# Kernel optimization log

Measured on AMD Instinct MI355X. Metric: run time of the kernel, lower is better.

## Reference

```python
import jax, jax.numpy as jnp
import numpy as np

N = 10000; E = 320000; NFEAT = 500; NHID = 256; C = 16; K = 64
GAMMA = 4; ALPHA = 0.1; BETA = 1.0; EPS = 0.1; LAMDA = 0.5; W1 = 0.5

def _init(key, shape, scale=0.05):
    return jax.random.normal(key, shape, dtype=jnp.float32) * scale

def setup_inputs():
    key = jax.random.key(0)
    ks = jax.random.split(key, 24)
    return {
        "x": jax.random.normal(ks[0], (N, NFEAT), dtype=jnp.float32),
        "edge_index": jax.random.randint(ks[1], (2, E), 0, N),
        "edge_weight": jax.random.uniform(ks[2], (E,), dtype=jnp.float32),
        "adj_weight": jax.random.uniform(ks[3], (E,), dtype=jnp.float32),
        "connect": jax.random.uniform(ks[4], (N, N), dtype=jnp.float32),
        "confidence_in": jax.random.uniform(ks[5], (2, E), dtype=jnp.float32),
        "lin1_w": _init(ks[6], (NHID, NFEAT)),
        "lin1_b": jnp.zeros((NHID,), jnp.float32),
        "lin2_w": _init(ks[7], (C, NHID)),
        "lin2_b": jnp.zeros((C,), jnp.float32),
        "lin_a_w": _init(ks[8], (NHID, N), 0.01),
        "lin_a_b": jnp.zeros((NHID,), jnp.float32),
        "lin_n_w": _init(ks[9], (C, C)),
        "lin_n_b": jnp.zeros((C,), jnp.float32),
        "left_w": _init(ks[10], (C, C)),
        "att_w": _init(ks[11], (1, C)),
        "v_w": _init(ks[12], (K, NHID)),
        "v_b": jnp.zeros((K,), jnp.float32),
        "W": _init(ks[13], (C, C)),
        "conf_param": jnp.zeros((3,), jnp.float32),
        "b_param": jnp.zeros((1,), jnp.float32),
    }

def _forward(x, edge_index, edge_weight, adj_weight, connect, confidence_in,
             lin1_w, lin1_b, lin2_w, lin2_b, lin_a_w, lin_a_b, lin_n_w, lin_n_b,
             left_w, att_w, v_w, v_b, W, conf_param, b_param):
    row, col = edge_index[0], edge_index[1]

    def spmm(vals, out_idx, M):
        # COO sparse @ dense: scatter-add per-edge vals * gathered rows of M
        return jax.ops.segment_sum(vals[:, None] * M, out_idx, num_segments=N)

    x_a = connect @ lin_a_w.T + lin_a_b            # [N, NHID]
    h = x @ lin1_w.T + lin1_b
    h = jax.nn.relu((1.0 - LAMDA) * h + LAMDA * x_a)
    raw = h                                        # [N, NHID]
    h = h @ lin2_w.T + lin2_b                      # [N, C]

    # neighbor label distribution: row-normalized adj @ one_hot(argmax softmax)
    y_hat = jnp.argmax(jax.nn.softmax(h, axis=1), axis=1)
    one_hot = jax.nn.one_hot(y_hat, C, dtype=h.dtype)
    nei = spmm(adj_weight, row, one_hot[col])
    s = nei.sum(axis=1, keepdims=True)
    nei = jnp.where(s != 0, nei / jnp.where(s == 0, 1.0, s), 0.0)

    x_n = jax.nn.relu(nei @ lin_n_w.T + lin_n_b)
    h = (1.0 - W1) * h + W1 * x_n
    init = h

    # per-edge attention-based confidence mixed with input confidences
    lx = h @ left_w.T
    confi = jax.nn.relu(lx[row] + lx[col])
    confi = jax.nn.sigmoid((confi @ att_w.T)[:, 0])
    w = jax.nn.softmax(conf_param)
    conf = confi * w[0] + confidence_in[0] * w[1] + confidence_in[1] * w[2]  # [E]

    V = raw @ v_w.T + v_b                          # [N, K]
    U = spmm(adj_weight, row, V[col]) @ jnp.linalg.inv(V.T @ V)
    eyeK = jnp.eye(K, dtype=h.dtype)

    def edge_mask_score(score):
        S = score ** 2
        ss = jnp.sort(S)
        q1, q3 = ss[E // 4], ss[3 * E // 4]
        thr = (q3 + 1.5 * (q3 - q1)) * conf        # [E]
        mask = (S < thr).astype(h.dtype)
        return (score + b_param[0]) * mask

    def update_u(U, V):
        SS = edge_mask_score(edge_weight - jnp.sum(U[row] * V[col], axis=1))
        temp = spmm(SS, row, V[col]) + U @ (V.T @ V) + EPS * (h @ (h.T @ V))
        inver = jnp.linalg.inv((1.0 + EPS) * (V.T @ V) + BETA * eyeK)
        return temp @ inver

    def update_v(U, V):
        SS = edge_mask_score(edge_weight - jnp.sum(V[row] * U[col], axis=1))
        # A^T @ U: scatter over col with U[row]
        temp = spmm(SS, col, U[row]) + V @ (U.T @ U) + EPS * (h @ (h.T @ U))
        inver = jnp.linalg.inv((1.0 + EPS) * (U.T @ U) + BETA * eyeK)
        return temp @ inver

    for j in range(GAMMA):
        if j % 2 == 0:
            U = update_u(U, V)
        else:
            V = update_v(U, V)

    prop = U @ (h.T @ V).T                         # [N, C]
    out = (1.0 - ALPHA) * prop + ALPHA * init
    return out @ W

def reference(x, edge_index, edge_weight, adj_weight, connect, confidence_in,
              lin1_w, lin1_b, lin2_w, lin2_b, lin_a_w, lin_a_b, lin_n_w, lin_n_b,
              left_w, att_w, v_w, v_b, W, conf_param, b_param):
    return _forward(x, edge_index, edge_weight, adj_weight, connect, confidence_in,
                    lin1_w, lin1_b, lin2_w, lin2_b, lin_a_w, lin_a_b, lin_n_w, lin_n_b,
                    left_w, att_w, v_w, v_b, W, conf_param, b_param)
```

## Files before the change

kernel.cpp:

```cpp
#include <hip/hip_runtime.h>
#include <cstddef>
#include <cstdint>


constexpr int kN  = 10000;
constexpr int kE  = 320000;
constexpr int kNH = 256;
constexpr int kC  = 16;
constexpr int kK  = 64;
constexpr int GRAM_PARTS = 256;
constexpr int PHASE_BLOCKS = 768;

struct SelState {
  int bin1[2]; int rem1[2];
};

typedef short bf16x8 __attribute__((ext_vector_type(8)));
typedef float f32x4 __attribute__((ext_vector_type(4)));
typedef ushort ushort8 __attribute__((ext_vector_type(8)));

__device__ __forceinline__ ushort f2bf(float x) {
  unsigned u = __float_as_uint(x);
  unsigned r = (u + 0x7fffu + ((u >> 16) & 1u)) >> 16;
  return (ushort)r;
}
__device__ __forceinline__ float bf2f(ushort h) {
  return __uint_as_float((unsigned)h << 16);
}
__device__ __forceinline__ int swz(int row, int byteInRow) {
  int chunk = (byteInRow >> 4) ^ ((row >> 1) & 3);
  return row * 64 + (chunk << 4) + (byteInRow & 15);
}

__global__ void split3_bf(const float* __restrict__ Wa, ushort* ha, ushort* la,
                          const float* __restrict__ Wx, ushort* hx, ushort* lx2,
                          const float* __restrict__ Wv, ushort* hv, ushort* lv)
{
  const int n1 = 256 * 10016, n2 = 256 * 512, n3 = 64 * 256;
  int t = blockIdx.x * 256 + threadIdx.x;
  if (t < n1) {
    int r = t / 10016, c = t % 10016;
    float v = (c < 10000) ? Wa[(size_t)r * 10000 + c] : 0.f;
    ushort h = f2bf(v); ha[t] = h; la[t] = f2bf(v - bf2f(h));
  } else if (t < n1 + n2) {
    int q = t - n1;
    int r = q / 512, c = q % 512;
    float v = (c < 500) ? Wx[(size_t)r * 500 + c] : 0.f;
    ushort h = f2bf(v); hx[q] = h; lx2[q] = f2bf(v - bf2f(h));
  } else if (t < n1 + n2 + n3) {
    int q = t - n1 - n2;
    float v = Wv[q];
    ushort h = f2bf(v); hv[q] = h; lv[q] = f2bf(v - bf2f(h));
  }
}

template<int BN, bool ALO>
__global__ __launch_bounds__(256) void gemm_v3(
    const float* __restrict__ A, const ushort* __restrict__ Bhg,
    const ushort* __restrict__ Blg, const float* __restrict__ bias,
    float* __restrict__ out, int M, int K, int Kp, int KR, int outStride)
{
  __shared__ __align__(16) char sAh[64 * 64];
  __shared__ __align__(16) char sAl[ALO ? 64 * 64 : 16];
  __shared__ __align__(16) char sBh[BN * 64];
  __shared__ __align__(16) char sBl[BN * 64];
  const int t = threadIdx.x;
  const int lane = t & 63, w = t >> 6;
  const int bm = blockIdx.x * 64;
  const int k0 = blockIdx.z * KR;
  const int kend = min(K, k0 + KR);
  out += (size_t)blockIdx.z * M * outStride;
  constexpr int WN = BN / 64;
  constexpr int RB = WN;
  const int wc = (w % WN) * 64;
  const int wr = (w / WN) * (RB * 16);
  const int l15 = lane & 15;
  const int lByte = (lane >> 4) * 16;
  const int ar = t >> 2, ac = t & 3;

  float pv[8];
  ushort8 pbh[WN], pbl[WN];

  {
    int gr = bm + ar, gk = k0 + ac * 8;
    if (gr < M && gk + 8 <= kend) {
      float4 v0 = *reinterpret_cast<const float4*>(A + (size_t)gr * K + gk);
      float4 v1 = *reinterpret_cast<const float4*>(A + (size_t)gr * K + gk + 4);
      pv[0] = v0.x; pv[1] = v0.y; pv[2] = v0.z; pv[3] = v0.w;
      pv[4] = v1.x; pv[5] = v1.y; pv[6] = v1.z; pv[7] = v1.w;
    } else {
#pragma unroll
      for (int q = 0; q < 8; q++)
        pv[q] = (gr < M && gk + q < kend) ? A[(size_t)gr * K + gk + q] : 0.f;
    }
#pragma unroll
    for (int i2 = 0; i2 < WN; i2++) {
      int idx = t + i2 * 256;
      int r = idx >> 2, c = idx & 3;
      size_t gb = (size_t)r * Kp + k0 + c * 8;
      pbh[i2] = *reinterpret_cast<const ushort8*>(Bhg + gb);
      pbl[i2] = *reinterpret_cast<const ushort8*>(Blg + gb);
    }
  }

  f32x4 acc[RB][4] = {};
  for (int kt = k0; kt < kend; kt += 32) {
    {
      ushort8 h8, l8;
#pragma unroll
      for (int q = 0; q < 8; q++) {
        ushort h = f2bf(pv[q]); h8[q] = h;
        if (ALO) l8[q] = f2bf(pv[q] - bf2f(h));
      }
      *reinterpret_cast<ushort8*>(sAh + swz(ar, ac * 16)) = h8;
      if (ALO) *reinterpret_cast<ushort8*>(sAl + swz(ar, ac * 16)) = l8;
#pragma unroll
      for (int i2 = 0; i2 < WN; i2++) {
        int idx = t + i2 * 256;
        int r = idx >> 2, c = idx & 3;
        *reinterpret_cast<ushort8*>(sBh + swz(r, c * 16)) = pbh[i2];
        *reinterpret_cast<ushort8*>(sBl + swz(r, c * 16)) = pbl[i2];
      }
    }
    __syncthreads();
    int kn = kt + 32;
    if (kn < kend) {
      int gr = bm + ar, gk = kn + ac * 8;
      if (gr < M && gk + 8 <= kend) {
        float4 v0 = *reinterpret_cast<const float4*>(A + (size_t)gr * K + gk);
        float4 v1 = *reinterpret_cast<const float4*>(A + (size_t)gr * K + gk + 4);
        pv[0] = v0.x; pv[1] = v0.y; pv[2] = v0.z; pv[3] = v0.w;
        pv[4] = v1.x; pv[5] = v1.y; pv[6] = v1.z; pv[7] = v1.w;
      } else {
#pragma unroll
        for (int q = 0; q < 8; q++)
          pv[q] = (gr < M && gk + q < kend) ? A[(size_t)gr * K + gk + q] : 0.f;
      }
#pragma unroll
      for (int i2 = 0; i2 < WN; i2++) {
        int idx = t + i2 * 256;
        int r = idx >> 2, c = idx & 3;
        size_t gb = (size_t)r * Kp + kn + c * 8;
        pbh[i2] = *reinterpret_cast<const ushort8*>(Bhg + gb);
        pbl[i2] = *reinterpret_cast<const ushort8*>(Blg + gb);
      }
    }
    bf16x8 bh[4], bl[4];
#pragma unroll
    for (int nbq = 0; nbq < 4; nbq++) {
      int rr = wc + nbq * 16 + l15;
      bh[nbq] = *reinterpret_cast<const bf16x8*>(sBh + swz(rr, lByte));
      bl[nbq] = *reinterpret_cast<const bf16x8*>(sBl + swz(rr, lByte));
    }
#pragma unroll
    for (int rb = 0; rb < RB; rb++) {
      int rr = wr + rb * 16 + l15;
      bf16x8 ah = *reinterpret_cast<const bf16x8*>(sAh + swz(rr, lByte));
#pragma unroll
      for (int nbq = 0; nbq < 4; nbq++) {
        acc[rb][nbq] = __builtin_amdgcn_mfma_f32_16x16x32_bf16(ah, bh[nbq], acc[rb][nbq], 0, 0, 0);
        acc[rb][nbq] = __builtin_amdgcn_mfma_f32_16x16x32_bf16(ah, bl[nbq], acc[rb][nbq], 0, 0, 0);
      }
      if (ALO) {
        bf16x8 al = *reinterpret_cast<const bf16x8*>(sAl + swz(rr, lByte));
#pragma unroll
        for (int nbq = 0; nbq < 4; nbq++)
          acc[rb][nbq] = __builtin_amdgcn_mfma_f32_16x16x32_bf16(al, bh[nbq], acc[rb][nbq], 0, 0, 0);
      }
    }
    __syncthreads();
  }
#pragma unroll
  for (int rb = 0; rb < RB; rb++) {
#pragma unroll
    for (int nbq = 0; nbq < 4; nbq++) {
      int colg = wc + nbq * 16 + l15;
      float bv = bias ? bias[colg] : 0.f;
#pragma unroll
      for (int jj = 0; jj < 4; jj++) {
        int rowg = bm + wr + rb * 16 + (lane >> 4) * 4 + jj;
        if (rowg < M) out[(size_t)rowg * outStride + colg] = acc[rb][nbq][jj] + bv;
      }
    }
  }
}

__global__ void reduce_raw(const float4* __restrict__ Pa, const float4* px,
                           const float* __restrict__ ba, const float* __restrict__ b1,
                           float4* rawOut, int* cntR, int* cntC, int* fillR,
                           int* fillC, float* nei)
{
  int t = blockIdx.x * 256 + threadIdx.x;
  if (t < kN) { cntR[t] = 0; cntC[t] = 0; fillR[t] = 0; fillC[t] = 0; }
  if (t < kN * kC) nei[t] = 0.f;
  if (t >= kN * kNH / 4) return;
  const int sl = kN * kNH / 4;
  float4 s = Pa[t];
#pragma unroll
  for (int p = 1; p < 6; p++) {
    float4 q = Pa[t + (size_t)p * sl];
    s.x += q.x; s.y += q.y; s.z += q.z; s.w += q.w;
  }
  float4 pxv = px[t];
  int c4 = t & 63;
  float4 vba = reinterpret_cast<const float4*>(ba)[c4];
  float4 vb1 = reinterpret_cast<const float4*>(b1)[c4];
  float4 r;
  r.x = fmaxf(0.5f * (s.x + vba.x) + 0.5f * (pxv.x + vb1.x), 0.f);
  r.y = fmaxf(0.5f * (s.y + vba.y) + 0.5f * (pxv.y + vb1.y), 0.f);
  r.z = fmaxf(0.5f * (s.z + vba.z) + 0.5f * (pxv.z + vb1.z), 0.f);
  r.w = fmaxf(0.5f * (s.w + vba.w) + 0.5f * (pxv.w + vb1.w), 0.f);
  rawOut[t] = r;
}

struct MegaArgs {
  const float* raw;
  const float* lin2_w; const float* lin2_b;
  const int* row; const int* col;
  const float* aw; const float* ew;
  const float* lnw; const float* lnb;
  const float* left_w; const float* att_w;
  const float* ci; const float* conf_p; const float* b_param;
  const float* Wm;
  float* h16; int* yhat; float* nei; float* hC; float* lx; float* conf;
  int* cntR; int* cntC; int* fillR; int* fillC; int* startR; int* startC;
  int* eR; int* eC; int* othR; int* othC;
  float* Va; float* Vb; float* Ua; float* Ub; float* T;
  float* score; float* G; float* Gi; float* Gp; float* hTX; float* Hp;
  int* hist1; int* h2a; int* h2b;
  float* P;
  SelState* sel;
  float* out;
};

__device__ __forceinline__ void uv_at(const MegaArgs& a, int j,
                                      float*& Ucur, float*& Unxt,
                                      float*& Vcur, float*& Vnxt)
{
  int uU = (j >= 1) + (j >= 3);
  int uV = (j >= 2) + (j >= 4);
  Ucur = (uU & 1) ? a.Ub : a.Ua; Unxt = (uU & 1) ? a.Ua : a.Ub;
  Vcur = (uV & 1) ? a.Vb : a.Va; Vnxt = (uV & 1) ? a.Va : a.Vb;
}

__device__ void gram2_dev(const float* M, const float* hc, float* P, int b, float* shm)
{
  float* sM = shm;
  float* sH = shm + 512;
  const int t = threadIdx.x;
  const int aG = t >> 2, cG0 = (t & 3) * 16;
  const int aH = t >> 4, cH0 = (t & 15) * 4;
  float accG[16]; float accH[4];
#pragma unroll
  for (int q = 0; q < 16; q++) accG[q] = 0.f;
#pragma unroll
  for (int q = 0; q < 4; q++) accH[q] = 0.f;
  int r0 = b * 40, r1 = min(kN, r0 + 40);
  for (int rb = r0; rb < r1; rb += 8) {
    int nb2 = min(8, r1 - rb);
    __syncthreads();
    for (int q = t; q < nb2 * 64; q += 256) sM[q] = M[(size_t)rb * 64 + q];
    for (int q = t; q < nb2 * 16; q += 256) sH[q] = hc[(size_t)rb * 16 + q];
    __syncthreads();
    for (int r = 0; r < nb2; r++) {
      float avG = sM[r * 64 + aG];
      const float* sbG = &sM[r * 64 + cG0];
#pragma unroll
      for (int q = 0; q < 16; q++) accG[q] += avG * sbG[q];
      float avH = sH[r * 16 + aH];
      const float* sbH = &sM[r * 64 + cH0];
#pragma unroll
      for (int q = 0; q < 4; q++) accH[q] += avH * sbH[q];
    }
  }
  float* p1 = P + (size_t)b * 5120 + aG * 64 + cG0;
#pragma unroll
  for (int q = 0; q < 16; q++) p1[q] = accG[q];
  float* p2 = P + (size_t)b * 5120 + 4096 + aH * 64 + cH0;
#pragma unroll
  for (int q = 0; q < 4; q++) p2[q] = accH[q];
}

__device__ void inverse_dev(const float* G, float* Gi, float alpha, float beta,
                            const float* hTX, float* Gp, float* Hp, float* shm)
{
  float* A = shm;
  float* prow = shm + 8448;
  float* fcol = shm + 8576;
  const int t = threadIdx.x;
  for (int q = t; q < 64 * 128; q += 256) {
    int r = q >> 7, c = q & 127;
    float v;
    if (c < 64) v = alpha * G[r * 64 + c] + ((c == r) ? beta : 0.f);
    else        v = (c - 64 == r) ? 1.f : 0.f;
    A[r * 132 + c] = v;
  }
  __syncthreads();
  const int i  = t >> 2;
  const int c0 = (t & 3) * 32;
  for (int k = 0; k < 64; k++) {
    if (t < 128) prow[t] = A[k * 132 + t];
    else if (t < 192) fcol[t - 128] = A[(t - 128) * 132 + k];
    __syncthreads();
    float pinv = 1.f / prow[k];
    float f = fcol[i];
    float4* Ar = reinterpret_cast<float4*>(&A[i * 132 + c0]);
    const float4* pr = reinterpret_cast<const float4*>(&prow[c0]);
    if (i == k) {
#pragma unroll
      for (int q = 0; q < 8; q++) {
        float4 p = pr[q];
        p.x *= pinv; p.y *= pinv; p.z *= pinv; p.w *= pinv;
        Ar[q] = p;
      }
    } else {
#pragma unroll
      for (int q = 0; q < 8; q++) {
        float4 p = pr[q]; float4 av = Ar[q];
        av.x -= f * (p.x * pinv); av.y -= f * (p.y * pinv);
        av.z -= f * (p.z * pinv); av.w -= f * (p.w * pinv);
        Ar[q] = av;
      }
    }
    __syncthreads();
  }
  for (int q = t; q < 4096; q += 256) Gi[q] = A[(q >> 6) * 132 + 64 + (q & 63)];
  if (Gp) {
    for (int q = t; q < 4096; q += 256) {
      int r = q >> 6, k = q & 63;
      float s = 0.f;
#pragma unroll 8
      for (int jj = 0; jj < 64; jj++) s += G[r * 64 + jj] * A[jj * 132 + 64 + k];
      Gp[q] = s;
    }
    for (int q = t; q < 1024; q += 256) {
      int c = q >> 6, k = q & 63;
      float s = 0.f;
#pragma unroll 8
      for (int jj = 0; jj < 64; jj++) s += hTX[c * 64 + jj] * A[jj * 132 + 64 + k];
      Hp[q] = 0.1f * s;
    }
  }
}

__device__ void scan_core(const int* H, int R, int* shm, int outSlot)
{
  const int t = threadIdx.x;
  int* part = shm;
  const int4* H4 = reinterpret_cast<const int4*>(H + t * 256);
  int lsum = 0;
  for (int b = 0; b < 64; b++) { int4 v = H4[b]; lsum += v.x + v.y + v.z + v.w; }
  part[t] = lsum;
  __syncthreads();
  for (int off = 1; off < 256; off <<= 1) {
    int v = part[t];
    int u = (t >= off) ? part[t - off] : 0;
    __syncthreads();
    part[t] = v + u;
    __syncthreads();
  }
  int cum = part[t] - lsum;
  int fb = -1, fr = 0;
  for (int b = 0; b < 64; b++) {
    int4 v = H4[b];
    int bb = t * 256 + b * 4;
    if (fb < 0 && R >= cum && R < cum + v.x) { fb = bb;     fr = R - cum; } cum += v.x;
    if (fb < 0 && R >= cum && R < cum + v.y) { fb = bb + 1; fr = R - cum; } cum += v.y;
    if (fb < 0 && R >= cum && R < cum + v.z) { fb = bb + 2; fr = R - cum; } cum += v.z;
    if (fb < 0 && R >= cum && R < cum + v.w) { fb = bb + 3; fr = R - cum; } cum += v.w;
  }
  if (fb >= 0) { shm[outSlot] = fb; shm[outSlot + 1] = fr; }
  __syncthreads();
}

__device__ void spmm_dev(const float* vals, const float* score, const float* conf,
                         float thr, float bp0,
                         const int* start, const int* eids, const int* oth,
                         const float* Msrc, float* T, int wid0, int wstride)
{
  int lane = threadIdx.x & 63;
  for (int wid = wid0; wid < kN; wid += wstride) {
    int p = start[wid], pend = start[wid + 1];
    float acc = 0.f;
    for (; p + 4 <= pend; p += 4) {
      int e0 = eids[p], e1 = eids[p + 1], e2 = eids[p + 2], e3 = eids[p + 3];
      int o0 = oth[p], o1 = oth[p + 1], o2 = oth[p + 2], o3 = oth[p + 3];
      float m0 = Msrc[(size_t)o0 * 64 + lane];
      float m1 = Msrc[(size_t)o1 * 64 + lane];
      float m2 = Msrc[(size_t)o2 * 64 + lane];
      float m3 = Msrc[(size_t)o3 * 64 + lane];
      float v0, v1, v2, v3;
      if (vals) { v0 = vals[e0]; v1 = vals[e1]; v2 = vals[e2]; v3 = vals[e3]; }
      else {
        float s0 = score[e0], s1 = score[e1], s2 = score[e2], s3 = score[e3];
        v0 = (s0 * s0 < thr * conf[e0]) ? (s0 + bp0) : 0.f;
        v1 = (s1 * s1 < thr * conf[e1]) ? (s1 + bp0) : 0.f;
        v2 = (s2 * s2 < thr * conf[e2]) ? (s2 + bp0) : 0.f;
        v3 = (s3 * s3 < thr * conf[e3]) ? (s3 + bp0) : 0.f;
      }
      acc += v0 * m0 + v1 * m1 + v2 * m2 + v3 * m3;
    }
    for (; p < pend; ++p) {
      int e = eids[p];
      float v;
      if (vals) v = vals[e];
      else { float sc = score[e]; v = (sc * sc < thr * conf[e]) ? (sc + bp0) : 0.f; }
      acc += v * Msrc[(size_t)oth[p] * 64 + lane];
    }
    T[(size_t)wid * 64 + lane] = acc;
  }
}

__device__ void outf_dev(const MegaArgs& a, const float* T, const float* X,
                         float* Out, int gtid, int gsz)
{
  for (int i = gtid; i < 65536; i += gsz) { a.hist1[i] = 0; a.h2a[i] = 0; a.h2b[i] = 0; }
  for (int t = gtid; t < kN * 16; t += gsz) {
    int i = t >> 4, kq = t & 15;
    const float* ti = T + (size_t)i * 64;
    const float4* G4 = reinterpret_cast<const float4*>(a.Gi);
    float4 s = make_float4(0.f, 0.f, 0.f, 0.f);
#pragma unroll 8
    for (int jj = 0; jj < 64; jj++) {
      float tv = ti[jj];
      float4 g = G4[jj * 16 + kq];
      s.x += tv * g.x; s.y += tv * g.y; s.z += tv * g.z; s.w += tv * g.w;
    }
    if (X) {
      const float* xi = X + (size_t)i * 64;
      const float4* Gp4 = reinterpret_cast<const float4*>(a.Gp);
      float4 s2 = make_float4(0.f, 0.f, 0.f, 0.f);
#pragma unroll 8
      for (int jj = 0; jj < 64; jj++) {
        float xv = xi[jj];
        float4 g = Gp4[jj * 16 + kq];
        s2.x += xv * g.x; s2.y += xv * g.y; s2.z += xv * g.z; s2.w += xv * g.w;
      }
      s.x += s2.x; s.y += s2.y; s.z += s2.z; s.w += s2.w;
      const float4* Hp4 = reinterpret_cast<const float4*>(a.Hp);
      float4 s3 = make_float4(0.f, 0.f, 0.f, 0.f);
#pragma unroll
      for (int c = 0; c < 16; c++) {
        float hv = a.hC[(size_t)i * 16 + c];
        float4 g = Hp4[c * 16 + kq];
        s3.x += hv * g.x; s3.y += hv * g.y; s3.z += hv * g.z; s3.w += hv * g.w;
      }
      s.x += s3.x; s.y += s3.y; s.z += s3.z; s.w += s3.w;
    }
    *reinterpret_cast<float4*>(Out + (size_t)i * 64 + kq * 4) = s;
  }
}

__device__ void reduce_dev(const MegaArgs& a, int gtid, int gsz)
{
  for (int c = gtid; c < 5120; c += gsz) {
    float s = 0.f;
    for (int p = 0; p < GRAM_PARTS; p++) s += a.P[(size_t)p * 5120 + c];
    if (c < 4096) a.G[c] = s;
    else a.hTX[c - 4096] = s;
  }
}

__global__ __launch_bounds__(256, 4) void mega_phase(MegaArgs a, int phase, int j)
{
  __shared__ __align__(16) float smem[8704];
  const int tid = threadIdx.x;
  const int bid = blockIdx.x;
  const int nb  = gridDim.x;
  const int gtid = bid * 256 + tid;
  const int gsz = nb * 256;
  float *Ucur, *Unxt, *Vcur, *Vnxt;
  uv_at(a, j, Ucur, Unxt, Vcur, Vnxt);
  bool up = ((j & 1) == 0);
  const float* Ma   = up ? Ucur : Vcur;
  const float* Mb   = up ? Vcur : Ucur;
  const float* Moth = up ? Vcur : Ucur;
  const float* Xcur = up ? Ucur : Vcur;
  float* Xout       = up ? Unxt : Vnxt;

  switch (phase) {
  case 0: {
    for (int t = gtid; t < kN * 16; t += gsz) {
      int i = t >> 4, jj = t & 15;
      const float4* av4 = reinterpret_cast<const float4*>(a.raw + (size_t)i * 256);
      const float4* bv4 = reinterpret_cast<const float4*>(a.lin2_w + (size_t)jj * 256);
      float s = a.lin2_b[jj];
#pragma unroll 8
      for (int q = 0; q < 64; q++) {
        float4 av = av4[q], bv = bv4[q];
        s += av.x * bv.x + av.y * bv.y + av.z * bv.z + av.w * bv.w;
      }
      a.h16[t] = s;
      float m = s; int am = jj;
#pragma unroll
      for (int off = 1; off < 16; off <<= 1) {
        float om = __shfl_xor(m, off);
        int oa = __shfl_xor(am, off);
        if (om > m || (om == m && oa < am)) { m = om; am = oa; }
      }
      if (jj == 0) a.yhat[i] = am;
    }
  } break;
  case 1: {
    for (int e = gtid; e < kE; e += gsz) {
      int r = a.row[e], c = a.col[e];
      atomicAdd(&a.cntR[r], 1);
      atomicAdd(&a.cntC[c], 1);
      atomicAdd(&a.nei[(size_t)r * 16 + a.yhat[c]], a.aw[e]);
    }
    for (int part = bid; part < GRAM_PARTS; part += nb)
      gram2_dev(a.Va, a.Va, a.P, part, smem);
  } break;
  case 2: {
    if (bid == 0) {
      int* part = (int*)smem;
      for (int pass = 0; pass < 2; ++pass) {
        const int* cnt = pass ? a.cntC : a.cntR;
        int* start = pass ? a.startC : a.startR;
        int bbase = tid * 40;
        int s = 0;
        for (int q = 0; q < 40; q++) { int idx = bbase + q; if (idx < kN) s += cnt[idx]; }
        part[tid] = s;
        __syncthreads();
        for (int off = 1; off < 256; off <<= 1) {
          int v = part[tid];
          int u = (tid >= off) ? part[tid - off] : 0;
          __syncthreads();
          part[tid] = v + u;
          __syncthreads();
        }
        int run = part[tid] - s;
        for (int q = 0; q < 40; q++) {
          int idx = bbase + q;
          if (idx < kN) { start[idx] = run; run += cnt[idx]; }
        }
        if (tid == 255) start[kN] = part[255];
        __syncthreads();
      }
    } else {
      int g2 = (bid - 1) * 256 + tid, s2 = (nb - 1) * 256;
      for (int i = g2; i < kN; i += s2) {
        float nv[16]; float s = 0.f;
#pragma unroll
        for (int c = 0; c < 16; c++) { nv[c] = a.nei[(size_t)i * 16 + c]; s += nv[c]; }
        float inv = (s != 0.f) ? 1.f / s : 0.f;
#pragma unroll
        for (int jj = 0; jj < 16; jj++) {
          float xn = a.lnb[jj];
#pragma unroll
          for (int c = 0; c < 16; c++) xn += (nv[c] * inv) * a.lnw[jj * 16 + c];
          xn = fmaxf(xn, 0.f);
          a.hC[(size_t)i * 16 + jj] = 0.5f * a.h16[(size_t)i * 16 + jj] + 0.5f * xn;
        }
      }
      for (int c = g2; c < 5120; c += s2) {
        float s = 0.f;
        for (int p = 0; p < GRAM_PARTS; p++) s += a.P[(size_t)p * 5120 + c];
        if (c < 4096) a.G[c] = s;
        else a.hTX[c - 4096] = s;
      }
    }
  } break;
  case 3: {
    if (bid == 0) {
      inverse_dev(a.G, a.Gi, 1.0f, 0.0f, nullptr, nullptr, nullptr, smem);
    } else {
      int g2 = (bid - 1) * 256 + tid, s2 = (nb - 1) * 256;
      for (int e = g2; e < kE; e += s2) {
        int r = a.row[e], c = a.col[e];
        int pr = a.startR[r] + atomicAdd(&a.fillR[r], 1);
        a.eR[pr] = e; a.othR[pr] = c;
        int pc = a.startC[c] + atomicAdd(&a.fillC[c], 1);
        a.eC[pc] = e; a.othC[pc] = r;
      }
      for (int t = g2; t < kN * 16; t += s2) {
        int i = t >> 4, jj = t & 15;
        float s = 0.f;
#pragma unroll
        for (int c = 0; c < 16; c++) s += a.hC[(size_t)i * 16 + c] * a.left_w[jj * 16 + c];
        a.lx[t] = s;
      }
    }
  } break;
  case 4: {
    for (int e = gtid; e < kE; e += gsz) {
      float p0 = a.conf_p[0], p1 = a.conf_p[1], p2 = a.conf_p[2];
      float m = fmaxf(p0, fmaxf(p1, p2));
      float e0 = expf(p0 - m), e1 = expf(p1 - m), e2 = expf(p2 - m);
      float inv = 1.f / (e0 + e1 + e2);
      float w0 = e0 * inv, w1 = e1 * inv, w2 = e2 * inv;
      const float* aa = a.lx + (size_t)a.row[e] * 16;
      const float* bb = a.lx + (size_t)a.col[e] * 16;
      float s = 0.f;
#pragma unroll
      for (int c = 0; c < 16; c++) s += fmaxf(aa[c] + bb[c], 0.f) * a.att_w[c];
      float cf = 1.f / (1.f + expf(-s));
      a.conf[e] = cf * w0 + a.ci[e] * w1 + a.ci[(size_t)kE + e] * w2;
    }
    spmm_dev(a.aw, nullptr, nullptr, 0.f, 0.f,
             a.startR, a.eR, a.othR, a.Va, a.T, bid * 4 + (tid >> 6), nb * 4);
  } break;
  case 5: outf_dev(a, a.T, nullptr, a.Ua, gtid, gsz); break;
  case 6: {
    for (int e = gtid; e < kE; e += gsz) {
      const float4* av4 = reinterpret_cast<const float4*>(Ma + (size_t)a.row[e] * 64);
      const float4* bv4 = reinterpret_cast<const float4*>(Mb + (size_t)a.col[e] * 64);
      float s = 0.f;
#pragma unroll
      for (int q = 0; q < 16; q++) {
        float4 av = av4[q], bv = bv4[q];
        s += av.x * bv.x + av.y * bv.y + av.z * bv.z + av.w * bv.w;
      }
      float sc = a.ew[e] - s;
      a.score[e] = sc;
      unsigned u = __float_as_uint(sc * sc);
      atomicAdd(&a.hist1[u >> 16], 1);
    }
    for (int part = bid; part < GRAM_PARTS; part += nb)
      gram2_dev(Moth, a.hC, a.P, part, smem);
  } break;
  case 7: {
    reduce_dev(a, gtid, gsz);
    int* ishm = (int*)smem;
    scan_core(a.hist1, kE / 4, ishm, 256);
    int b0 = ishm[256];
    if (bid == 0 && tid == 0) { a.sel->bin1[0] = ishm[256]; a.sel->rem1[0] = ishm[257]; }
    scan_core(a.hist1, 3 * kE / 4, ishm, 258);
    int b1 = ishm[258];
    if (bid == 0 && tid == 0) { a.sel->bin1[1] = ishm[258]; a.sel->rem1[1] = ishm[259]; }
    for (int e = gtid; e < kE; e += gsz) {
      float sc = a.score[e];
      unsigned u = __float_as_uint(sc * sc);
      int top = (int)(u >> 16);
      if (top == b0) atomicAdd(&a.h2a[u & 0xFFFF], 1);
      if (top == b1) atomicAdd(&a.h2b[u & 0xFFFF], 1);
    }
  } break;
  case 8: {
    if (bid == 0) {
      inverse_dev(a.G, a.Gi, 1.1f, 1.0f, a.hTX, a.Gp, a.Hp, smem);
    } else {
      int* ishm = (int*)smem;
      int bA = a.sel->bin1[0], bB = a.sel->bin1[1];
      int rA = a.sel->rem1[0], rB = a.sel->rem1[1];
      scan_core(a.h2a, rA, ishm, 256);
      int f0 = ishm[256];
      scan_core(a.h2b, rB, ishm, 258);
      int f1 = ishm[258];
      float q1 = __uint_as_float(((unsigned)bA << 16) | (unsigned)f0);
      float q3 = __uint_as_float(((unsigned)bB << 16) | (unsigned)f1);
      float thr = q3 + 1.5f * (q3 - q1);
      float bp0 = a.b_param[0];
      if (up) spmm_dev(nullptr, a.score, a.conf, thr, bp0,
                       a.startR, a.eR, a.othR, Vcur, a.T,
                       (bid - 1) * 4 + (tid >> 6), (nb - 1) * 4);
      else    spmm_dev(nullptr, a.score, a.conf, thr, bp0,
                       a.startC, a.eC, a.othC, Ucur, a.T,
                       (bid - 1) * 4 + (tid >> 6), (nb - 1) * 4);
    }
  } break;
  case 9: outf_dev(a, a.T, Xcur, Xout, gtid, gsz); break;
  case 10: {
    for (int part = bid; part < GRAM_PARTS; part += nb)
      gram2_dev(Vcur, a.hC, a.P, part, smem);
  } break;
  case 11: reduce_dev(a, gtid, gsz); break;
  case 12: {
    float* sh = smem;
    float* sW = smem + 1024;
    for (int q = tid; q < 1024; q += 256) sh[q] = a.hTX[q];
    sW[tid] = a.Wm[tid & 255];
    __syncthreads();
    for (int i = gtid; i < kN; i += gsz) {
      const float* u = Ucur + (size_t)i * 64;
      float pre[16];
#pragma unroll
      for (int c = 0; c < 16; c++) {
        float s = 0.f;
#pragma unroll
        for (int k = 0; k < 64; k++) s += u[k] * sh[c * 64 + k];
        pre[c] = 0.9f * s + 0.1f * a.hC[(size_t)i * 16 + c];
      }
#pragma unroll
      for (int jj = 0; jj < 16; jj++) {
        float o = 0.f;
#pragma unroll
        for (int c = 0; c < 16; c++) o += pre[c] * sW[c * 16 + jj];
        a.out[(size_t)i * 16 + jj] = o;
      }
    }
  } break;
  }
}

extern "C" void kernel_launch(void* const* d_in, const int* in_sizes, int n_in,
                              void* d_out, int out_size, void* d_ws, size_t ws_size,
                              hipStream_t stream)
{
  const float* x       = (const float*)d_in[0];
  const int*   eidx    = (const int*)d_in[1];
  const float* ew      = (const float*)d_in[2];
  const float* aw      = (const float*)d_in[3];
  const float* connect = (const float*)d_in[4];
  const float* ci      = (const float*)d_in[5];
  const float* lin1_w  = (const float*)d_in[6];
  const float* lin1_b  = (const float*)d_in[7];
  const float* lin2_w  = (const float*)d_in[8];
  const float* lin2_b  = (const float*)d_in[9];
  const float* lin_a_w = (const float*)d_in[10];
  const float* lin_a_b = (const float*)d_in[11];
  const float* lin_n_w = (const float*)d_in[12];
  const float* lin_n_b = (const float*)d_in[13];
  const float* left_w  = (const float*)d_in[14];
  const float* att_w   = (const float*)d_in[15];
  const float* v_w     = (const float*)d_in[16];
  const float* v_b     = (const float*)d_in[17];
  const float* Wm      = (const float*)d_in[18];
  const float* conf_p  = (const float*)d_in[19];
  const float* b_param = (const float*)d_in[20];
  const int* row = eidx;
  const int* col = eidx + kE;
  float* out = (float*)d_out;

  char* base = (char*)d_ws;
  size_t off = 0;
  auto alloc = [&](size_t bytes) -> void* {
    void* p = base + off;
    off += bytes;
    off = (off + 255) & ~(size_t)255;
    return p;
  };
  float* raw   = (float*)alloc((size_t)kN * kNH * 4);
  float* h16   = (float*)alloc((size_t)kN * kC * 4);
  float* hC    = (float*)alloc((size_t)kN * kC * 4);
  float* nei   = (float*)alloc((size_t)kN * kC * 4);
  float* lx    = (float*)alloc((size_t)kN * kC * 4);
  int*   yhat  = (int*)alloc((size_t)kN * 4);
  float* conf  = (float*)alloc((size_t)kE * 4);
  float* Va    = (float*)alloc((size_t)kN * kK * 4);
  float* Vb    = (float*)alloc((size_t)kN * kK * 4);
  float* Ua    = (float*)alloc((size_t)kN * kK * 4);
  float* Ub    = (float*)alloc((size_t)kN * kK * 4);
  float* T     = (float*)alloc((size_t)kN * kK * 4);
  float* score = (float*)alloc((size_t)kE * 4);
  float* G     = (float*)alloc(64 * 64 * 4);
  float* Gi    = (float*)alloc(64 * 64 * 4);
  float* Gp    = (float*)alloc(64 * 64 * 4);
  float* hTX   = (float*)alloc(kC * kK * 4);
  float* Hp    = (float*)alloc(kC * kK * 4);
  int* hist1   = (int*)alloc(65536 * 4);
  int* h2a     = (int*)alloc(65536 * 4);
  int* h2b     = (int*)alloc(65536 * 4);
  SelState* sel = (SelState*)alloc(sizeof(SelState));
  int* cntR    = (int*)alloc((size_t)kN * 4);
  int* cntC    = (int*)alloc((size_t)kN * 4);
  int* fillR   = (int*)alloc((size_t)kN * 4);
  int* fillC   = (int*)alloc((size_t)kN * 4);
  int* startR  = (int*)alloc((size_t)(kN + 1) * 4);
  int* startC  = (int*)alloc((size_t)(kN + 1) * 4);
  int* eR      = (int*)alloc((size_t)kE * 4);
  int* eC      = (int*)alloc((size_t)kE * 4);
  int* othR    = (int*)alloc((size_t)kE * 4);
  int* othC    = (int*)alloc((size_t)kE * 4);
  float* P     = (float*)alloc((size_t)GRAM_PARTS * 5120 * 4);
  const int KpC = 10016, KpX = 512, KpV = 256;
  ushort* BcH = (ushort*)alloc((size_t)256 * KpC * 2);
  ushort* BcL = (ushort*)alloc((size_t)256 * KpC * 2);
  ushort* BxH = (ushort*)alloc((size_t)256 * KpX * 2);
  ushort* BxL = (ushort*)alloc((size_t)256 * KpX * 2);
  ushort* BvH = (ushort*)alloc((size_t)64 * KpV * 2);
  ushort* BvL = (ushort*)alloc((size_t)64 * KpV * 2);
  float* Pbig  = (float*)alloc((size_t)6 * kN * kNH * 4);

  {
    int total = 256 * KpC + 256 * KpX + 64 * KpV;
    split3_bf<<<(total + 255) / 256, 256, 0, stream>>>(
        lin_a_w, BcH, BcL, lin1_w, BxH, BxL, v_w, BvH, BvL);
  }

  gemm_v3<256, false><<<dim3(157, 1, 6), 256, 0, stream>>>(
      connect, BcH, BcL, nullptr, Pbig, kN, 10000, KpC, 1696, kNH);
  gemm_v3<256, true><<<dim3(157, 1, 1), 256, 0, stream>>>(
      x, BxH, BxL, nullptr, raw, kN, 500, KpX, 512, kNH);
  reduce_raw<<<(kN * kNH / 4 + 255) / 256, 256, 0, stream>>>(
      (const float4*)Pbig, (const float4*)raw, lin_a_b, lin1_b, (float4*)raw,
      cntR, cntC, fillR, fillC, nei);
  gemm_v3<64, true><<<dim3(157, 1, 1), 256, 0, stream>>>(
      raw, BvH, BvL, v_b, Va, kN, 256, KpV, 256, kK);

  MegaArgs ma;
  ma.raw = raw; ma.lin2_w = lin2_w; ma.lin2_b = lin2_b;
  ma.row = row; ma.col = col; ma.aw = aw; ma.ew = ew;
  ma.lnw = lin_n_w; ma.lnb = lin_n_b; ma.left_w = left_w; ma.att_w = att_w;
  ma.ci = ci; ma.conf_p = conf_p; ma.b_param = b_param; ma.Wm = Wm;
  ma.h16 = h16; ma.yhat = yhat; ma.nei = nei; ma.hC = hC; ma.lx = lx; ma.conf = conf;
  ma.cntR = cntR; ma.cntC = cntC; ma.fillR = fillR; ma.fillC = fillC;
  ma.startR = startR; ma.startC = startC;
  ma.eR = eR; ma.eC = eC; ma.othR = othR; ma.othC = othC;
  ma.Va = Va; ma.Vb = Vb; ma.Ua = Ua; ma.Ub = Ub; ma.T = T;
  ma.score = score; ma.G = G; ma.Gi = Gi; ma.Gp = Gp; ma.hTX = hTX; ma.Hp = Hp;
  ma.hist1 = hist1; ma.h2a = h2a; ma.h2b = h2b;
  ma.P = P; ma.sel = sel; ma.out = out;

  const dim3 pg(PHASE_BLOCKS);
  for (int p = 0; p <= 5; p++) mega_phase<<<pg, 256, 0, stream>>>(ma, p, 0);
  for (int j = 0; j < 4; j++)
    for (int p = 6; p <= 9; p++) mega_phase<<<pg, 256, 0, stream>>>(ma, p, j);
  mega_phase<<<pg, 256, 0, stream>>>(ma, 10, 4);
  mega_phase<<<pg, 256, 0, stream>>>(ma, 11, 4);
  mega_phase<<<pg, 256, 0, stream>>>(ma, 12, 4);
}
```

Baseline: 2.490 ms.

## Use two-level coarse histograms for quantile select; drop GEMM register prefetch

Adds 256-bin coarse histograms alongside the 65536-bin ones, so the quantile search first scans the coarse bins and then only one 256-entry fine slice. Previously every block in the phase read the full 64K histogram twice per scan. The cost is an extra atomic per edge into a small, highly contended coarse histogram. Separately, the GEMM drops its register double-buffer prefetch of the A and B tiles and loads each tile directly before the sync, which lowers register pressure but gives up load/compute overlap.

```diff
diff --git a/kernel.cpp b/kernel.cpp
--- a/kernel.cpp
+++ b/kernel.cpp
@@ -78,73 +78,41 @@
   const int lByte = (lane >> 4) * 16;
   const int ar = t >> 2, ac = t & 3;
 
-  float pv[8];
-  ushort8 pbh[WN], pbl[WN];
-
-  {
-    int gr = bm + ar, gk = k0 + ac * 8;
-    if (gr < M && gk + 8 <= kend) {
-      float4 v0 = *reinterpret_cast<const float4*>(A + (size_t)gr * K + gk);
-      float4 v1 = *reinterpret_cast<const float4*>(A + (size_t)gr * K + gk + 4);
-      pv[0] = v0.x; pv[1] = v0.y; pv[2] = v0.z; pv[3] = v0.w;
-      pv[4] = v1.x; pv[5] = v1.y; pv[6] = v1.z; pv[7] = v1.w;
-    } else {
-#pragma unroll
-      for (int q = 0; q < 8; q++)
-        pv[q] = (gr < M && gk + q < kend) ? A[(size_t)gr * K + gk + q] : 0.f;
-    }
-#pragma unroll
-    for (int i2 = 0; i2 < WN; i2++) {
-      int idx = t + i2 * 256;
-      int r = idx >> 2, c = idx & 3;
-      size_t gb = (size_t)r * Kp + k0 + c * 8;
-      pbh[i2] = *reinterpret_cast<const ushort8*>(Bhg + gb);
-      pbl[i2] = *reinterpret_cast<const ushort8*>(Blg + gb);
-    }
-  }
-
   f32x4 acc[RB][4] = {};
   for (int kt = k0; kt < kend; kt += 32) {
     {
-      ushort8 h8, l8;
-#pragma unroll
-      for (int q = 0; q < 8; q++) {
-        ushort h = f2bf(pv[q]); h8[q] = h;
-        if (ALO) l8[q] = f2bf(pv[q] - bf2f(h));
-      }
-      *reinterpret_cast<ushort8*>(sAh + swz(ar, ac * 16)) = h8;
-      if (ALO) *reinterpret_cast<ushort8*>(sAl + swz(ar, ac * 16)) = l8;
-#pragma unroll
-      for (int i2 = 0; i2 < WN; i2++) {
-        int idx = t + i2 * 256;
-        int r = idx >> 2, c = idx & 3;
-        *reinterpret_cast<ushort8*>(sBh + swz(r, c * 16)) = pbh[i2];
-        *reinterpret_cast<ushort8*>(sBl + swz(r, c * 16)) = pbl[i2];
-      }
-    }
-    __syncthreads();
-    int kn = kt + 32;
-    if (kn < kend) {
-      int gr = bm + ar, gk = kn + ac * 8;
+      int gr = bm + ar, gk = kt + ac * 8;
+      float v[8];
       if (gr < M && gk + 8 <= kend) {
         float4 v0 = *reinterpret_cast<const float4*>(A + (size_t)gr * K + gk);
         float4 v1 = *reinterpret_cast<const float4*>(A + (size_t)gr * K + gk + 4);
-        pv[0] = v0.x; pv[1] = v0.y; pv[2] = v0.z; pv[3] = v0.w;
-        pv[4] = v1.x; pv[5] = v1.y; pv[6] = v1.z; pv[7] = v1.w;
+        v[0] = v0.x; v[1] = v0.y; v[2] = v0.z; v[3] = v0.w;
+        v[4] = v1.x; v[5] = v1.y; v[6] = v1.z; v[7] = v1.w;
       } else {
 #pragma unroll
         for (int q = 0; q < 8; q++)
-          pv[q] = (gr < M && gk + q < kend) ? A[(size_t)gr * K + gk + q] : 0.f;
-      }
-#pragma unroll
-      for (int i2 = 0; i2 < WN; i2++) {
-        int idx = t + i2 * 256;
-        int r = idx >> 2, c = idx & 3;
-        size_t gb = (size_t)r * Kp + kn + c * 8;
-        pbh[i2] = *reinterpret_cast<const ushort8*>(Bhg + gb);
-        pbl[i2] = *reinterpret_cast<const ushort8*>(Blg + gb);
-      }
-    }
+          v[q] = (gr < M && gk + q < kend) ? A[(size_t)gr * K + gk + q] : 0.f;
+      }
+      ushort8 h8, l8;
+#pragma unroll
+      for (int q = 0; q < 8; q++) {
+        ushort h = f2bf(v[q]); h8[q] = h;
+        if (ALO) l8[q] = f2bf(v[q] - bf2f(h));
+      }
+      *reinterpret_cast<ushort8*>(sAh + swz(ar, ac * 16)) = h8;
+      if (ALO) *reinterpret_cast<ushort8*>(sAl + swz(ar, ac * 16)) = l8;
+    }
+#pragma unroll
+    for (int i2 = 0; i2 < BN / 64; i2++) {
+      int idx = t + i2 * 256;
+      int r = idx >> 2, c = idx & 3;
+      size_t gb = (size_t)r * Kp + kt + c * 8;
+      ushort8 hv = *reinterpret_cast<const ushort8*>(Bhg + gb);
+      ushort8 lv = *reinterpret_cast<const ushort8*>(Blg + gb);
+      *reinterpret_cast<ushort8*>(sBh + swz(r, c * 16)) = hv;
+      *reinterpret_cast<ushort8*>(sBl + swz(r, c * 16)) = lv;
+    }
+    __syncthreads();
     bf16x8 bh[4], bl[4];
 #pragma unroll
     for (int nbq = 0; nbq < 4; nbq++) {
@@ -228,6 +196,7 @@
   float* Va; float* Vb; float* Ua; float* Ub; float* T;
   float* score; float* G; float* Gi; float* Gp; float* hTX; float* Hp;
   int* hist1; int* h2a; int* h2b;
+  int* hist1C; int* h2aC; int* h2bC;
   float* P;
   SelState* sel;
   float* out;
@@ -343,14 +312,14 @@
   }
 }
 
-__device__ void scan_core(const int* H, int R, int* shm, int outSlot)
+__device__ void hscan(const int* __restrict__ Hc, const int* __restrict__ Hf,
+                      int R, int* shm, int outSlot)
 {
   const int t = threadIdx.x;
   int* part = shm;
-  const int4* H4 = reinterpret_cast<const int4*>(H + t * 256);
-  int lsum = 0;
-  for (int b = 0; b < 64; b++) { int4 v = H4[b]; lsum += v.x + v.y + v.z + v.w; }
-  part[t] = lsum;
+  int c = Hc[t];
+  __syncthreads();
+  part[t] = c;
   __syncthreads();
   for (int off = 1; off < 256; off <<= 1) {
     int v = part[t];
@@ -359,17 +328,23 @@
     part[t] = v + u;
     __syncthreads();
   }
-  int cum = part[t] - lsum;
-  int fb = -1, fr = 0;
-  for (int b = 0; b < 64; b++) {
-    int4 v = H4[b];
-    int bb = t * 256 + b * 4;
-    if (fb < 0 && R >= cum && R < cum + v.x) { fb = bb;     fr = R - cum; } cum += v.x;
-    if (fb < 0 && R >= cum && R < cum + v.y) { fb = bb + 1; fr = R - cum; } cum += v.y;
-    if (fb < 0 && R >= cum && R < cum + v.z) { fb = bb + 2; fr = R - cum; } cum += v.z;
-    if (fb < 0 && R >= cum && R < cum + v.w) { fb = bb + 3; fr = R - cum; } cum += v.w;
-  }
-  if (fb >= 0) { shm[outSlot] = fb; shm[outSlot + 1] = fr; }
+  int cum = part[t] - c;
+  if (R >= cum && R < cum + c) { shm[outSlot + 2] = t; shm[outSlot + 3] = R - cum; }
+  __syncthreads();
+  int cb = shm[outSlot + 2], rem = shm[outSlot + 3];
+  int f = Hf[cb * 256 + t];
+  __syncthreads();
+  part[t] = f;
+  __syncthreads();
+  for (int off = 1; off < 256; off <<= 1) {
+    int v = part[t];
+    int u = (t >= off) ? part[t - off] : 0;
+    __syncthreads();
+    part[t] = v + u;
+    __syncthreads();
+  }
+  int cum2 = part[t] - f;
+  if (rem >= cum2 && rem < cum2 + f) { shm[outSlot] = cb * 256 + t; shm[outSlot + 1] = rem - cum2; }
   __syncthreads();
 }
 
@@ -415,6 +390,7 @@
                          float* Out, int gtid, int gsz)
 {
   for (int i = gtid; i < 65536; i += gsz) { a.hist1[i] = 0; a.h2a[i] = 0; a.h2b[i] = 0; }
+  if (gtid < 256) { a.hist1C[gtid] = 0; a.h2aC[gtid] = 0; a.h2bC[gtid] = 0; }
   for (int t = gtid; t < kN * 16; t += gsz) {
     int i = t >> 4, kq = t & 15;
     const float* ti = T + (size_t)i * 64;
@@ -615,6 +591,7 @@
       a.score[e] = sc;
       unsigned u = __float_as_uint(sc * sc);
       atomicAdd(&a.hist1[u >> 16], 1);
+      atomicAdd(&a.hist1C[u >> 24], 1);
     }
     for (int part = bid; part < GRAM_PARTS; part += nb)
       gram2_dev(Moth, a.hC, a.P, part, smem);
@@ -622,18 +599,18 @@
   case 7: {
     reduce_dev(a, gtid, gsz);
     int* ishm = (int*)smem;
-    scan_core(a.hist1, kE / 4, ishm, 256);
-    int b0 = ishm[256];
-    if (bid == 0 && tid == 0) { a.sel->bin1[0] = ishm[256]; a.sel->rem1[0] = ishm[257]; }
-    scan_core(a.hist1, 3 * kE / 4, ishm, 258);
-    int b1 = ishm[258];
-    if (bid == 0 && tid == 0) { a.sel->bin1[1] = ishm[258]; a.sel->rem1[1] = ishm[259]; }
+    hscan(a.hist1C, a.hist1, kE / 4, ishm, 260);
+    int b0 = ishm[260];
+    if (bid == 0 && tid == 0) { a.sel->bin1[0] = ishm[260]; a.sel->rem1[0] = ishm[261]; }
+    hscan(a.hist1C, a.hist1, 3 * kE / 4, ishm, 264);
+    int b1 = ishm[264];
+    if (bid == 0 && tid == 0) { a.sel->bin1[1] = ishm[264]; a.sel->rem1[1] = ishm[265]; }
     for (int e = gtid; e < kE; e += gsz) {
       float sc = a.score[e];
       unsigned u = __float_as_uint(sc * sc);
       int top = (int)(u >> 16);
-      if (top == b0) atomicAdd(&a.h2a[u & 0xFFFF], 1);
-      if (top == b1) atomicAdd(&a.h2b[u & 0xFFFF], 1);
+      if (top == b0) { atomicAdd(&a.h2a[u & 0xFFFF], 1); atomicAdd(&a.h2aC[(u >> 8) & 0xFF], 1); }
+      if (top == b1) { atomicAdd(&a.h2b[u & 0xFFFF], 1); atomicAdd(&a.h2bC[(u >> 8) & 0xFF], 1); }
     }
   } break;
   case 8: {
@@ -643,10 +620,10 @@
       int* ishm = (int*)smem;
       int bA = a.sel->bin1[0], bB = a.sel->bin1[1];
       int rA = a.sel->rem1[0], rB = a.sel->rem1[1];
-      scan_core(a.h2a, rA, ishm, 256);
-      int f0 = ishm[256];
-      scan_core(a.h2b, rB, ishm, 258);
-      int f1 = ishm[258];
+      hscan(a.h2aC, a.h2a, rA, ishm, 260);
+      int f0 = ishm[260];
+      hscan(a.h2bC, a.h2b, rB, ishm, 264);
+      int f1 = ishm[264];
       float q1 = __uint_as_float(((unsigned)bA << 16) | (unsigned)f0);
       float q3 = __uint_as_float(((unsigned)bB << 16) | (unsigned)f1);
       float thr = q3 + 1.5f * (q3 - q1);
@@ -751,6 +728,9 @@
   int* hist1   = (int*)alloc(65536 * 4);
   int* h2a     = (int*)alloc(65536 * 4);
   int* h2b     = (int*)alloc(65536 * 4);
+  int* hist1C  = (int*)alloc(256 * 4);
+  int* h2aC    = (int*)alloc(256 * 4);
+  int* h2bC    = (int*)alloc(256 * 4);
   SelState* sel = (SelState*)alloc(sizeof(SelState));
   int* cntR    = (int*)alloc((size_t)kN * 4);
   int* cntC    = (int*)alloc((size_t)kN * 4);
@@ -800,6 +780,7 @@
   ma.Va = Va; ma.Vb = Vb; ma.Ua = Ua; ma.Ub = Ub; ma.T = T;
   ma.score = score; ma.G = G; ma.Gi = Gi; ma.Gp = Gp; ma.hTX = hTX; ma.Hp = Hp;
   ma.hist1 = hist1; ma.h2a = h2a; ma.h2b = h2b;
+  ma.hist1C = hist1C; ma.h2aC = h2aC; ma.h2bC = h2bC;
   ma.P = P; ma.sel = sel; ma.out = out;
 
   const dim3 pg(PHASE_BLOCKS);
```

New measurement: 8.596 ms. 3.45x slower.
